# Performance work log

Hardware: AMD Instinct MI355X
Metric: run time of the kernel (lower is better)

Reference implementation:

```python
import jax, jax.numpy as jnp
import numpy as np

EMBED_DIM = 768
NUM_HEADS = 12
NUM_BOND_TYPES = 4
NEG_INF = -1e9


def setup_inputs() -> dict:
    key = jax.random.key(0)
    ks = jax.random.split(key, 8)
    B, N, E = 32, 512, EMBED_DIM
    x = jax.random.normal(ks[0], (B, N, E), dtype=jnp.float32)
    adj = jax.random.randint(ks[1], (B, N, N), 0, 2, dtype=jnp.int32)
    bond = jax.random.randint(ks[2], (B, N, N), 0, NUM_BOND_TYPES + 1, dtype=jnp.int32)
    # nn.Linear(E, 3E): weight (3E, E), bias (3E)
    lim_qkv = 1.0 / np.sqrt(E)
    qkv_w = jax.random.uniform(ks[3], (3 * E, E), minval=-lim_qkv, maxval=lim_qkv, dtype=jnp.float32)
    qkv_b = jax.random.uniform(ks[4], (3 * E,), minval=-lim_qkv, maxval=lim_qkv, dtype=jnp.float32)
    out_w = jax.random.uniform(ks[5], (E, E), minval=-lim_qkv, maxval=lim_qkv, dtype=jnp.float32)
    out_b = jax.random.uniform(ks[6], (E,), minval=-lim_qkv, maxval=lim_qkv, dtype=jnp.float32)
    # nn.Embedding(num_bond_types+1, 1), padding_idx=0 -> row 0 is zero
    bond_table = jax.random.normal(ks[7], (NUM_BOND_TYPES + 1, 1), dtype=jnp.float32)
    bond_table = bond_table.at[0].set(0.0)
    return {"x": x, "adj": adj, "bond": bond, "num_heads": NUM_HEADS,
            "qkv_w": qkv_w, "qkv_b": qkv_b, "out_w": out_w, "out_b": out_b,
            "bond_table": bond_table}


def reference(x, adj, bond, num_heads, qkv_w, qkv_b, out_w, out_b, bond_table):
    B, N, E = x.shape
    hd = E // num_heads
    scale = hd ** -0.5
    # enforce padding_idx=0 semantics
    bond_table = bond_table.at[0].set(0.0)
    qkv = x @ qkv_w.T + qkv_b                      # (B, N, 3E)
    qkv = qkv.reshape(B, N, 3, num_heads, hd).transpose(2, 0, 3, 1, 4)
    q, k, v = qkv[0], qkv[1], qkv[2]               # (B, h, N, hd)
    attn = jnp.einsum('bhnd,bhmd->bhnm', q, k) * scale
    attn = attn + adj.astype(x.dtype)[:, None, :, :]
    bond_bias = bond_table[bond, 0]                # (B, N, N) embedding gather
    attn = attn + bond_bias[:, None, :, :]
    attn = jnp.where(attn == 0, NEG_INF, attn)     # masked_fill(attn == 0)
    attn = jax.nn.softmax(attn, axis=-1)
    out = jnp.einsum('bhnm,bhmd->bhnd', attn, v)   # (B, h, N, hd)
    out = out.transpose(0, 2, 1, 3).reshape(B, N, E)
    return out @ out_w.T + out_b
```

## Files before the change

### kernel.cpp

```cpp
#include <hip/hip_runtime.h>
#include <hip/hip_bf16.h>

typedef __attribute__((ext_vector_type(8))) short short8;
typedef __attribute__((ext_vector_type(4))) float f32x4;
typedef __attribute__((ext_vector_type(4))) unsigned int uint4v;
typedef __attribute__((ext_vector_type(4))) int int4v;

#define MFMA16(a,b,c) __builtin_amdgcn_mfma_f32_16x16x32_bf16((a),(b),(c),0,0,0)

#define GLOAD_LDS16(g, l) \
    __builtin_amdgcn_global_load_lds((const __attribute__((address_space(1))) void*)(g), \
                                     (__attribute__((address_space(3))) void*)(l), 16, 0, 0)

__device__ __forceinline__ unsigned short f2bf(float f){
    union { float f; unsigned int u; } c; c.f = f;
    unsigned int u = c.u;
    u = (u + 0x7fffu + ((u >> 16) & 1u)) >> 16;
    return (unsigned short)u;
}
__device__ __forceinline__ float bf2f(unsigned short s){
    union { unsigned int u; float f; } c; c.u = ((unsigned int)s) << 16;
    return c.f;
}

__device__ __forceinline__ void tsplit(float f, unsigned short &h, unsigned short &l){
    unsigned int u = __builtin_bit_cast(unsigned int, f);
    float hi = __builtin_bit_cast(float, u & 0xffff0000u);
    h = (unsigned short)(u >> 16);
    l = (unsigned short)(__builtin_bit_cast(unsigned int, f - hi) >> 16);
}


__global__ void pack_x_kernel(const float* __restrict__ x, unsigned int* __restrict__ img){
    int tid = blockIdx.x * 256 + threadIdx.x;
    int m = tid / 96, grp = tid - m * 96;
    const float* src = x + (size_t)m * 768 + grp * 8;
    f32x4 v0 = ((const f32x4*)src)[0];
    f32x4 v1 = ((const f32x4*)src)[1];
    short8 h8, l8;
    #pragma unroll
    for (int j = 0; j < 4; ++j){
        unsigned short hh, ll;
        tsplit(v0[j], hh, ll); h8[j]   = (short)hh; l8[j]   = (short)ll;
        tsplit(v1[j], hh, ll); h8[4+j] = (short)hh; l8[4+j] = (short)ll;
    }
    int mt = m >> 7, row = m & 127, kt = grp >> 2, gi = grp & 3;
    int sw = (row & 7) << 4;
    char* bp = (char*)img + ((size_t)(mt*24 + kt))*16384 + row*128;
    *(short8*)(bp + ((gi*32     ) ^ sw)) = h8;
    *(short8*)(bp + ((gi*32 + 16) ^ sw)) = l8;
}

__global__ void pack_w_kernel(const float* __restrict__ wsrc, unsigned int* __restrict__ img, int total){
    int tid = blockIdx.x * 256 + threadIdx.x;
    if (tid >= total) return;
    int n = tid / 96, grp = tid - n * 96;
    const float* src = wsrc + (size_t)n * 768 + grp * 8;
    f32x4 v0 = ((const f32x4*)src)[0];
    f32x4 v1 = ((const f32x4*)src)[1];
    short8 h8, l8;
    #pragma unroll
    for (int j = 0; j < 4; ++j){
        unsigned short hh = f2bf(v0[j]);
        h8[j] = (short)hh; l8[j] = (short)f2bf(v0[j] - bf2f(hh));
        hh = f2bf(v1[j]);
        h8[4+j] = (short)hh; l8[4+j] = (short)f2bf(v1[j] - bf2f(hh));
    }
    int jt = n >> 7, row = n & 127, kt = grp >> 2, gi = grp & 3;
    int sw = (row & 7) << 4;
    char* bp = (char*)img + ((size_t)(jt*24 + kt))*16384 + row*128;
    *(short8*)(bp + ((gi*32     ) ^ sw)) = h8;
    *(short8*)(bp + ((gi*32 + 16) ^ sw)) = l8;
}

__global__ void bias_kernel(const int* __restrict__ adj, const int* __restrict__ bond,
                            const float* __restrict__ table, float* __restrict__ biasC, int n4){
    int i = blockIdx.x * 256 + threadIdx.x;
    if (i >= n4) return;
    int4v a  = ((const int4v*)adj)[i];
    int4v bd = ((const int4v*)bond)[i];
    const float t1 = table[1], t2 = table[2], t3 = table[3], t4 = table[4];
    f32x4 o;
    #pragma unroll
    for (int j = 0; j < 4; ++j){
        int bv = bd[j];
        float tb = (bv == 1) ? t1 : (bv == 2) ? t2 : (bv == 3) ? t3 : (bv == 4) ? t4 : 0.0f;
        o[j] = (float)a[j] + tb;
    }
    ((f32x4*)biasC)[i] = o;
}

template<int EMODE>
__global__ __launch_bounds__(256, 3)
void gemm_img(const unsigned int* __restrict__ Aimg, const unsigned int* __restrict__ Bimg,
              const float* __restrict__ bias, int NT, int RPX,
              float* __restrict__ C, int N,
              char* __restrict__ qo, char* __restrict__ ko, char* __restrict__ vo)
{
    __shared__ unsigned int lds[8192];

    const int lin = blockIdx.x;
    const int xcd = lin & 7, idx = lin >> 3;
    const int grp  = idx / (RPX * 6);
    const int rem  = idx - grp * (RPX * 6);
    const int rowL = rem / 6, c6 = rem - rowL * 6;
    const int colT = grp * 6 + c6;
    const int mt = xcd * RPX + rowL;
    const int m0 = mt << 7, j0 = colT << 7;

    const int t = threadIdx.x, l = t & 63, w = t >> 6;
    const int c = l & 15, g = l >> 4;
    const int wr = (w >> 1) * 64, wc2 = (w & 1) * 64;

    const unsigned int* Ablk = Aimg + (size_t)mt   * NT * 4096;
    const unsigned int* Bblk = Bimg + (size_t)colT * NT * 4096;

    f32x4 acc[4][4] = {};

    for (int kt = 0; kt < NT; ++kt){
        const unsigned int* As = Ablk + kt*4096 + t*4;
        const unsigned int* Bs = Bblk + kt*4096 + t*4;
        unsigned int* Ad = lds + t*4;
        unsigned int* Bd = lds + 4096 + t*4;
        #pragma unroll
        for (int i = 0; i < 4; ++i){
            GLOAD_LDS16(As + i*1024, Ad + i*1024);
            GLOAD_LDS16(Bs + i*1024, Bd + i*1024);
        }
        __syncthreads();

        short8 bh[4], bl[4];
        #pragma unroll
        for (int fc = 0; fc < 4; ++fc){
            int row = wc2 + fc*16 + c;
            int sw = (row & 7) << 4;
            const char* p = (const char*)(lds + 4096) + row*128;
            bh[fc] = *(const short8*)(p + ((g*32     ) ^ sw));
            bl[fc] = *(const short8*)(p + ((g*32 + 16) ^ sw));
        }
        #pragma unroll
        for (int fr = 0; fr < 4; ++fr){
            int row = wr + fr*16 + c;
            int sw = (row & 7) << 4;
            const char* p = (const char*)lds + row*128;
            short8 ah = *(const short8*)(p + ((g*32     ) ^ sw));
            short8 al = *(const short8*)(p + ((g*32 + 16) ^ sw));
            __builtin_amdgcn_s_setprio(1);
            #pragma unroll
            for (int fc = 0; fc < 4; ++fc){
                acc[fr][fc] = MFMA16(ah, bh[fc], acc[fr][fc]);
                acc[fr][fc] = MFMA16(ah, bl[fc], acc[fr][fc]);
                acc[fr][fc] = MFMA16(al, bh[fc], acc[fr][fc]);
            }
            __builtin_amdgcn_s_setprio(0);
        }
        __syncthreads();
    }

    #pragma unroll
    for (int fr = 0; fr < 4; ++fr){
        #pragma unroll
        for (int fc = 0; fc < 4; ++fc){
            #pragma unroll
            for (int r = 0; r < 4; ++r){
                int m = m0 + wr + fr*16 + g*4 + r;
                int j = j0 + wc2 + fc*16 + c;
                float val = acc[fr][fc][r] + bias[j];
                if constexpr (EMODE == 0){
                    C[(size_t)m * N + j] = val;
                } else {
                    int sec = j / 768;
                    int off = j - sec * 768;
                    int head = off >> 6, d = off & 63;
                    int bb = m >> 9, n = m & 511;
                    int bh2 = bb * 12 + head;
                    unsigned short hh, ll;
                    tsplit(val, hh, ll);
                    if (sec == 0) {
                        char* p = qo + ((size_t)bh2*512 + n)*256 + (d>>3)*32 + (d&7)*2;
                        *(unsigned short*)(p     ) = hh;
                        *(unsigned short*)(p + 16) = ll;
                    } else if (sec == 1) {
                        int row = n & 63;
                        int ksw = (((row & 7) + (((row >> 3) & 3) << 1)) & 7) << 4;
                        char* p = ko + (size_t)(bh2*8 + (n>>6))*16384 + row*256;
                        *(unsigned short*)(p + ((((d>>3)*32)     ) ^ ksw) + (d&7)*2) = hh;
                        *(unsigned short*)(p + ((((d>>3)*32) + 16) ^ ksw) + (d&7)*2) = ll;
                    } else {
                        int col = n & 63, sw = (d & 7) << 4;
                        char* p = vo + (size_t)(bh2*8 + (n>>6))*16384 + d*256;
                        *(unsigned short*)(p + ((((col>>3)*32)     ) ^ sw) + (col&7)*2) = hh;
                        *(unsigned short*)(p + ((((col>>3)*32) + 16) ^ sw) + (col&7)*2) = ll;
                    }
                }
            }
        }
    }
}

__global__ __launch_bounds__(256, 4)
void attn_kernel(const char* __restrict__ qb,
                 const unsigned int* __restrict__ kimg,
                 const unsigned int* __restrict__ vimg,
                 const float* __restrict__ biasC,
                 char* __restrict__ oimg)
{
    __shared__ unsigned int Kt[4096];
    __shared__ unsigned int Vt[4096];

    const int lin = blockIdx.x;
    const int xcd = lin & 7, m_ = lin >> 3;
    const int bgrp = m_ / 96, r_ = m_ - bgrp * 96;
    const int b = (bgrp << 3) | xcd;
    const int h = r_ >> 3, qt = r_ & 7;
    const int bh = b * 12 + h, q0 = qt * 64;

    const int t = threadIdx.x, l = t & 63, w = t >> 6;
    const int c = l & 15, g = l >> 4;

    short8 qh[2], ql[2];
    {
        int qrow = q0 + w*16 + c;
        const char* qp = qb + ((size_t)bh*512 + qrow)*256;
        #pragma unroll
        for (int ks = 0; ks < 2; ++ks){
            qh[ks] = *(const short8*)(qp + ks*128 + g*32);
            ql[ks] = *(const short8*)(qp + ks*128 + g*32 + 16);
        }
    }

    f32x4 O[4] = {};
    float m_run = -3e38f, l_run = 0.0f;

    const float* biasRow = biasC + ((size_t)b * 512 + (q0 + w*16 + c)) * 512;

    for (int kt = 0; kt < 8; ++kt){
        {
            const unsigned int* kg = kimg + (size_t)(bh*8 + kt)*4096 + t*4;
            const unsigned int* vg = vimg + (size_t)(bh*8 + kt)*4096 + t*4;
            #pragma unroll
            for (int i = 0; i < 4; ++i){
                GLOAD_LDS16(kg + i*1024, &Kt[t*4 + i*1024]);
                GLOAD_LDS16(vg + i*1024, &Vt[t*4 + i*1024]);
            }
        }

        f32x4 bia[4];
        #pragma unroll
        for (int fc = 0; fc < 4; ++fc){
            int keyb = kt*64 + (fc>>1)*32 + g*8 + ((fc&1)<<2);
            bia[fc] = *(const f32x4*)(biasRow + keyb);
        }
        __syncthreads();

        f32x4 S[4] = {};
        #pragma unroll
        for (int fc = 0; fc < 4; ++fc){
            int row = (fc>>1)*32 + ((c>>2)<<3) + ((fc&1)<<2) + (c&3);
            int ksw = (((row & 7) + (((row >> 3) & 3) << 1)) & 7) << 4;
            const char* kp = (const char*)Kt + row*256;
            short8 kbh0 = *(const short8*)(kp + ((g*32           ) ^ ksw));
            short8 kbl0 = *(const short8*)(kp + ((g*32 + 16      ) ^ ksw));
            short8 kbh1 = *(const short8*)(kp + ((128 + g*32     ) ^ ksw));
            short8 kbl1 = *(const short8*)(kp + ((128 + g*32 + 16) ^ ksw));
            __builtin_amdgcn_s_setprio(1);
            S[fc] = MFMA16(kbh0, qh[0], S[fc]);
            S[fc] = MFMA16(kbl0, qh[0], S[fc]);
            S[fc] = MFMA16(kbh0, ql[0], S[fc]);
            S[fc] = MFMA16(kbh1, qh[1], S[fc]);
            S[fc] = MFMA16(kbl1, qh[1], S[fc]);
            S[fc] = MFMA16(kbh1, ql[1], S[fc]);
            __builtin_amdgcn_s_setprio(0);
        }

        float p[4][4];
        float pmax = -3e38f;
        #pragma unroll
        for (int fc = 0; fc < 4; ++fc){
            #pragma unroll
            for (int r = 0; r < 4; ++r){
                float val = fmaf(S[fc][r], 0.125f, bia[fc][r]);
                if (val == 0.0f) val = -1e9f;
                p[fc][r] = val;
                pmax = fmaxf(pmax, val);
            }
        }
        pmax = fmaxf(pmax, __shfl_xor(pmax, 16));
        pmax = fmaxf(pmax, __shfl_xor(pmax, 32));
        float mn = fmaxf(m_run, pmax);
        float corr = __expf(m_run - mn);
        float rs = 0.0f;
        #pragma unroll
        for (int fc = 0; fc < 4; ++fc){
            #pragma unroll
            for (int r = 0; r < 4; ++r){
                float e = __expf(p[fc][r] - mn);
                p[fc][r] = e;
                rs += e;
            }
        }
        rs += __shfl_xor(rs, 16);
        rs += __shfl_xor(rs, 32);
        l_run = l_run * corr + rs;
        m_run = mn;

        #pragma unroll
        for (int r = 0; r < 4; ++r){
            float cr = __shfl(corr, (l & 48) | (g*4 + r));
            O[0][r] *= cr; O[1][r] *= cr; O[2][r] *= cr; O[3][r] *= cr;
        }

        #pragma unroll
        for (int ks = 0; ks < 2; ++ks){
            uint4v ph, plo;
            #pragma unroll
            for (int j = 0; j < 4; ++j){
                const int fc = 2*ks + (j >> 1);
                const int r0 = (j & 1) * 2;
                float a  = p[fc][r0], bq = p[fc][r0 + 1];
                unsigned int ua = __builtin_bit_cast(unsigned int, a);
                unsigned int ub = __builtin_bit_cast(unsigned int, bq);
                float ra = a  - __builtin_bit_cast(float, ua & 0xffff0000u);
                float rb = bq - __builtin_bit_cast(float, ub & 0xffff0000u);
                ph[j]  = __builtin_amdgcn_perm(ub, ua, 0x07060302u);
                plo[j] = __builtin_amdgcn_perm(__builtin_bit_cast(unsigned int, rb),
                                               __builtin_bit_cast(unsigned int, ra), 0x07060302u);
            }
            short8 pah = __builtin_bit_cast(short8, ph);
            short8 pal = __builtin_bit_cast(short8, plo);
            #pragma unroll
            for (int hf = 0; hf < 4; ++hf){
                int row = hf*16 + c;
                int sw = (row & 7) << 4;
                const char* vp = (const char*)Vt + row*256;
                short8 vbh = *(const short8*)(vp + ((ks*128 + g*32     ) ^ sw));
                short8 vbl = *(const short8*)(vp + ((ks*128 + g*32 + 16) ^ sw));
                __builtin_amdgcn_s_setprio(1);
                O[hf] = MFMA16(pah, vbh, O[hf]);
                O[hf] = MFMA16(pah, vbl, O[hf]);
                O[hf] = MFMA16(pal, vbh, O[hf]);
                __builtin_amdgcn_s_setprio(0);
            }
        }
        __syncthreads();
    }

    float linv = 1.0f / l_run;
    #pragma unroll
    for (int r = 0; r < 4; ++r){
        float inv = __shfl(linv, (l & 48) | (g*4 + r));
        int m = b*512 + q0 + w*16 + g*4 + r;
        int mt = m >> 7, mrow2 = m & 127;
        int swz = (mrow2 & 7) << 4;
        char* rowp = oimg + ((size_t)mt*24)*16384 + (size_t)mrow2*128;
        #pragma unroll
        for (int hf = 0; hf < 4; ++hf){
            int e = h*64 + hf*16 + c;
            int kt2 = e >> 5, gi = (e >> 3) & 3, pos = e & 7;
            unsigned short hh, ll;
            tsplit(O[hf][r] * inv, hh, ll);
            char* pp = rowp + (size_t)kt2*16384;
            *(unsigned short*)(pp + (((gi*32)     ) ^ swz) + pos*2) = hh;
            *(unsigned short*)(pp + (((gi*32) + 16) ^ swz) + pos*2) = ll;
        }
    }
}

extern "C" void kernel_launch(void* const* d_in, const int* in_sizes, int n_in,
                              void* d_out, int out_size, void* d_ws, size_t ws_size,
                              hipStream_t stream)
{
    const float* x     = (const float*)d_in[0];
    const int*   adj   = (const int*)d_in[1];
    const int*   bond  = (const int*)d_in[2];
    const float* qkv_w = (const float*)d_in[4];
    const float* qkv_b = (const float*)d_in[5];
    const float* out_w = (const float*)d_in[6];
    const float* out_b = (const float*)d_in[7];
    const float* btab  = (const float*)d_in[8];
    float* out = (float*)d_out;

    const size_t QKV = 12582912;
    unsigned int* q   = (unsigned int*)d_ws;
    unsigned int* k   = q  + QKV;
    unsigned int* vt  = k  + QKV;
    unsigned int* r1  = vt + QKV;
    unsigned int* w2i = r1 + QKV;
    unsigned int* r2  = w2i + 589824;
    unsigned int* w1i = r2;
    float* biasC      = (float*)r2;

    dim3 blk(256);
    pack_w_kernel<<<dim3(864), blk, 0, stream>>>(qkv_w, w1i, 2304*96);
    pack_w_kernel<<<dim3(288), blk, 0, stream>>>(out_w, w2i, 768*96);
    pack_x_kernel<<<dim3(6144), blk, 0, stream>>>(x, r1);

    gemm_img<1><<<dim3(2304), blk, 0, stream>>>(r1, w1i, qkv_b, 24, 16,
                                                nullptr, 2304, (char*)q, (char*)k, (char*)vt);

    bias_kernel<<<dim3(8192), blk, 0, stream>>>(adj, bond, btab, biasC, (32*512*512)/4);

    attn_kernel<<<dim3(3072), blk, 0, stream>>>((const char*)q, k, vt, biasC, (char*)r1);

    gemm_img<0><<<dim3(768), blk, 0, stream>>>(r1, w2i, out_b, 24, 16,
                                               out, 768, nullptr, nullptr, nullptr);
}
```

Baseline: 389.3 us.

## Enlarge GEMM tiles to 256x256 with 512 threads and double-buffered LDS prefetch

Reworks the split-bf16 GEMM kernel to use 256x256 output tiles per 512-thread block with 128KB of dynamic LDS. The next K-tile is loaded into a second buffer while the current one is consumed by MFMAs, interleaved across four sub-phases with barriers. The aim is to hide global-to-LDS latency and raise data reuse per load. In exchange, occupancy drops to one block per CU and register pressure rises from the 8x4 accumulator array. The grid is also much smaller (576 and 192 blocks), which risks poor CU fill for the output projection.

```diff
diff --git a/kernel.cpp b/kernel.cpp
--- a/kernel.cpp
+++ b/kernel.cpp
@@ -91,80 +91,117 @@
 }
 
 template<int EMODE>
-__global__ __launch_bounds__(256, 3)
+__global__ __launch_bounds__(512, 1)
 void gemm_img(const unsigned int* __restrict__ Aimg, const unsigned int* __restrict__ Bimg,
-              const float* __restrict__ bias, int NT, int RPX,
+              const float* __restrict__ bias, int NT, int NCOL,
               float* __restrict__ C, int N,
               char* __restrict__ qo, char* __restrict__ ko, char* __restrict__ vo)
 {
-    __shared__ unsigned int lds[8192];
+    extern __shared__ unsigned int lds[];
 
     const int lin = blockIdx.x;
     const int xcd = lin & 7, idx = lin >> 3;
-    const int grp  = idx / (RPX * 6);
-    const int rem  = idx - grp * (RPX * 6);
-    const int rowL = rem / 6, c6 = rem - rowL * 6;
-    const int colT = grp * 6 + c6;
-    const int mt = xcd * RPX + rowL;
-    const int m0 = mt << 7, j0 = colT << 7;
+    const int rowL = idx / NCOL, colT = idx - rowL * NCOL;
+    const int bm = xcd * 8 + rowL;
+    const int m0 = bm << 8, j0 = colT << 8;
 
     const int t = threadIdx.x, l = t & 63, w = t >> 6;
     const int c = l & 15, g = l >> 4;
-    const int wr = (w >> 1) * 64, wc2 = (w & 1) * 64;
-
-    const unsigned int* Ablk = Aimg + (size_t)mt   * NT * 4096;
-    const unsigned int* Bblk = Bimg + (size_t)colT * NT * 4096;
-
-    f32x4 acc[4][4] = {};
+    const int wr2 = (w >> 2) * 128;
+    const int wc4 = (w & 3) * 64;
+
+    const unsigned int* Ab0 = Aimg + (size_t)(bm*2    ) * NT * 4096;
+    const unsigned int* Ab1 = Aimg + (size_t)(bm*2 + 1) * NT * 4096;
+    const unsigned int* Bb0 = Bimg + (size_t)(colT*2    ) * NT * 4096;
+    const unsigned int* Bb1 = Bimg + (size_t)(colT*2 + 1) * NT * 4096;
+
+    const int Aoff = (w >> 2) * 16384;
+    const int Boff = (2 + ((w & 3) >> 1)) * 16384;
+    const int rBbase = (w & 1) * 64;
+
+    f32x4 acc[8][4] = {};
+
+    {
+        const unsigned int* s0 = Ab0 + t*4;
+        const unsigned int* s1 = Ab1 + t*4;
+        const unsigned int* s2 = Bb0 + t*4;
+        const unsigned int* s3 = Bb1 + t*4;
+        unsigned int* d = lds + t*4;
+        GLOAD_LDS16(s0,        d        ); GLOAD_LDS16(s0 + 2048, d + 2048 );
+        GLOAD_LDS16(s1,        d + 4096 ); GLOAD_LDS16(s1 + 2048, d + 6144 );
+        GLOAD_LDS16(s2,        d + 8192 ); GLOAD_LDS16(s2 + 2048, d + 10240);
+        GLOAD_LDS16(s3,        d + 12288); GLOAD_LDS16(s3 + 2048, d + 14336);
+    }
+    asm volatile("s_waitcnt vmcnt(0)" ::: "memory");
+    __builtin_amdgcn_s_barrier();
 
     for (int kt = 0; kt < NT; ++kt){
-        const unsigned int* As = Ablk + kt*4096 + t*4;
-        const unsigned int* Bs = Bblk + kt*4096 + t*4;
-        unsigned int* Ad = lds + t*4;
-        unsigned int* Bd = lds + 4096 + t*4;
-        #pragma unroll
-        for (int i = 0; i < 4; ++i){
-            GLOAD_LDS16(As + i*1024, Ad + i*1024);
-            GLOAD_LDS16(Bs + i*1024, Bd + i*1024);
-        }
-        __syncthreads();
+        const char* bufb = (const char*)lds + (kt & 1) * 65536;
+        unsigned int* bufn = lds + ((kt & 1) ^ 1) * 16384;
+        const bool pre = (kt + 1 < NT);
 
         short8 bh[4], bl[4];
         #pragma unroll
+        for (int p = 0; p < 4; ++p){
+            short8 ah[2], al[2];
+            #pragma unroll
+            for (int i = 0; i < 2; ++i){
+                int r = (2*p + i)*16 + c;
+                int sw = (r & 7) << 4;
+                const char* pa = bufb + Aoff + r*128;
+                ah[i] = *(const short8*)(pa + ((g*32     ) ^ sw));
+                al[i] = *(const short8*)(pa + ((g*32 + 16) ^ sw));
+            }
+            if (p == 0){
+                #pragma unroll
+                for (int fc = 0; fc < 4; ++fc){
+                    int r = rBbase + fc*16 + c;
+                    int sw = (r & 7) << 4;
+                    const char* pb = bufb + Boff + r*128;
+                    bh[fc] = *(const short8*)(pb + ((g*32     ) ^ sw));
+                    bl[fc] = *(const short8*)(pb + ((g*32 + 16) ^ sw));
+                }
+                if (pre){
+                    const unsigned int* s0 = Ab0 + (kt+1)*4096 + t*4;
+                    const unsigned int* s1 = Ab1 + (kt+1)*4096 + t*4;
+                    unsigned int* d = bufn + t*4;
+                    GLOAD_LDS16(s0,        d       ); GLOAD_LDS16(s0 + 2048, d + 2048);
+                    GLOAD_LDS16(s1,        d + 4096); GLOAD_LDS16(s1 + 2048, d + 6144);
+                }
+            }
+            if (p == 1 && pre){
+                const unsigned int* s2 = Bb0 + (kt+1)*4096 + t*4;
+                const unsigned int* s3 = Bb1 + (kt+1)*4096 + t*4;
+                unsigned int* d = bufn + t*4;
+                GLOAD_LDS16(s2,        d + 8192 ); GLOAD_LDS16(s2 + 2048, d + 10240);
+                GLOAD_LDS16(s3,        d + 12288); GLOAD_LDS16(s3 + 2048, d + 14336);
+            }
+            __builtin_amdgcn_s_barrier();
+            __builtin_amdgcn_s_setprio(1);
+            #pragma unroll
+            for (int i = 0; i < 2; ++i){
+                #pragma unroll
+                for (int fc = 0; fc < 4; ++fc){
+                    acc[2*p+i][fc] = MFMA16(ah[i], bh[fc], acc[2*p+i][fc]);
+                    acc[2*p+i][fc] = MFMA16(ah[i], bl[fc], acc[2*p+i][fc]);
+                    acc[2*p+i][fc] = MFMA16(al[i], bh[fc], acc[2*p+i][fc]);
+                }
+            }
+            __builtin_amdgcn_s_setprio(0);
+            if (p == 3)
+                asm volatile("s_waitcnt vmcnt(0)" ::: "memory");
+            __builtin_amdgcn_s_barrier();
+        }
+    }
+
+    #pragma unroll
+    for (int fr = 0; fr < 8; ++fr){
+        #pragma unroll
         for (int fc = 0; fc < 4; ++fc){
-            int row = wc2 + fc*16 + c;
-            int sw = (row & 7) << 4;
-            const char* p = (const char*)(lds + 4096) + row*128;
-            bh[fc] = *(const short8*)(p + ((g*32     ) ^ sw));
-            bl[fc] = *(const short8*)(p + ((g*32 + 16) ^ sw));
-        }
-        #pragma unroll
-        for (int fr = 0; fr < 4; ++fr){
-            int row = wr + fr*16 + c;
-            int sw = (row & 7) << 4;
-            const char* p = (const char*)lds + row*128;
-            short8 ah = *(const short8*)(p + ((g*32     ) ^ sw));
-            short8 al = *(const short8*)(p + ((g*32 + 16) ^ sw));
-            __builtin_amdgcn_s_setprio(1);
-            #pragma unroll
-            for (int fc = 0; fc < 4; ++fc){
-                acc[fr][fc] = MFMA16(ah, bh[fc], acc[fr][fc]);
-                acc[fr][fc] = MFMA16(ah, bl[fc], acc[fr][fc]);
-                acc[fr][fc] = MFMA16(al, bh[fc], acc[fr][fc]);
-            }
-            __builtin_amdgcn_s_setprio(0);
-        }
-        __syncthreads();
-    }
-
-    #pragma unroll
-    for (int fr = 0; fr < 4; ++fr){
-        #pragma unroll
-        for (int fc = 0; fc < 4; ++fc){
             #pragma unroll
             for (int r = 0; r < 4; ++r){
-                int m = m0 + wr + fr*16 + g*4 + r;
-                int j = j0 + wc2 + fc*16 + c;
+                int m = m0 + wr2 + fr*16 + g*4 + r;
+                int j = j0 + wc4 + fc*16 + c;
                 float val = acc[fr][fc][r] + bias[j];
                 if constexpr (EMODE == 0){
                     C[(size_t)m * N + j] = val;
@@ -395,13 +432,13 @@
     pack_w_kernel<<<dim3(288), blk, 0, stream>>>(out_w, w2i, 768*96);
     pack_x_kernel<<<dim3(6144), blk, 0, stream>>>(x, r1);
 
-    gemm_img<1><<<dim3(2304), blk, 0, stream>>>(r1, w1i, qkv_b, 24, 16,
-                                                nullptr, 2304, (char*)q, (char*)k, (char*)vt);
+    gemm_img<1><<<dim3(576), dim3(512), 131072, stream>>>(
+        r1, w1i, qkv_b, 24, 9, nullptr, 2304, (char*)q, (char*)k, (char*)vt);
 
     bias_kernel<<<dim3(8192), blk, 0, stream>>>(adj, bond, btab, biasC, (32*512*512)/4);
 
     attn_kernel<<<dim3(3072), blk, 0, stream>>>((const char*)q, k, vt, biasC, (char*)r1);
 
-    gemm_img<0><<<dim3(768), blk, 0, stream>>>(r1, w2i, out_b, 24, 16,
-                                               out, 768, nullptr, nullptr, nullptr);
-}
+    gemm_img<0><<<dim3(192), dim3(512), 131072, stream>>>(
+        r1, w2i, out_b, 24, 3, out, 768, nullptr, nullptr, nullptr);
+}
```

New measurement: 444.7 us. 14.2% more time.

## Process 128 query rows per attention block to reuse K/V tiles

Applied to the files above, without the earlier changes.

Each attention workgroup now handles 128 queries instead of 64: every wave processes two 16-row query sub-tiles against the same K/V LDS tiles, which halves the number of blocks and the total K/V global-to-LDS traffic and sync count. Register pressure rises (double S, O, P state), so attention's launch bound drops to 3 waves per SIMD, while the GEMM's bound is raised to 4. The swapped occupancy hints may trade spills or latency hiding against the reuse gain.

```diff
diff --git a/kernel.cpp b/kernel.cpp
--- a/kernel.cpp
+++ b/kernel.cpp
@@ -91,7 +91,7 @@
 }
 
 template<int EMODE>
-__global__ __launch_bounds__(256, 3)
+__global__ __launch_bounds__(256, 4)
 void gemm_img(const unsigned int* __restrict__ Aimg, const unsigned int* __restrict__ Bimg,
               const float* __restrict__ bias, int NT, int RPX,
               float* __restrict__ C, int N,
@@ -198,7 +198,7 @@
     }
 }
 
-__global__ __launch_bounds__(256, 4)
+__global__ __launch_bounds__(256, 3)
 void attn_kernel(const char* __restrict__ qb,
                  const unsigned int* __restrict__ kimg,
                  const unsigned int* __restrict__ vimg,
@@ -210,29 +210,32 @@
 
     const int lin = blockIdx.x;
     const int xcd = lin & 7, m_ = lin >> 3;
-    const int bgrp = m_ / 96, r_ = m_ - bgrp * 96;
+    const int bgrp = m_ / 48, r_ = m_ - bgrp * 48;
     const int b = (bgrp << 3) | xcd;
-    const int h = r_ >> 3, qt = r_ & 7;
-    const int bh = b * 12 + h, q0 = qt * 64;
+    const int h = r_ >> 2, qt = r_ & 3;
+    const int bh = b * 12 + h, q0 = qt * 128;
 
     const int t = threadIdx.x, l = t & 63, w = t >> 6;
     const int c = l & 15, g = l >> 4;
 
-    short8 qh[2], ql[2];
-    {
-        int qrow = q0 + w*16 + c;
+    short8 qh[2][2], ql[2][2];
+    #pragma unroll
+    for (int qk = 0; qk < 2; ++qk){
+        int qrow = q0 + w*32 + qk*16 + c;
         const char* qp = qb + ((size_t)bh*512 + qrow)*256;
         #pragma unroll
         for (int ks = 0; ks < 2; ++ks){
-            qh[ks] = *(const short8*)(qp + ks*128 + g*32);
-            ql[ks] = *(const short8*)(qp + ks*128 + g*32 + 16);
-        }
-    }
-
-    f32x4 O[4] = {};
-    float m_run = -3e38f, l_run = 0.0f;
-
-    const float* biasRow = biasC + ((size_t)b * 512 + (q0 + w*16 + c)) * 512;
+            qh[qk][ks] = *(const short8*)(qp + ks*128 + g*32);
+            ql[qk][ks] = *(const short8*)(qp + ks*128 + g*32 + 16);
+        }
+    }
+
+    f32x4 O[2][4] = {};
+    float m_run[2] = {-3e38f, -3e38f};
+    float l_run[2] = {0.f, 0.f};
+
+    const float* biasRow0 = biasC + ((size_t)b * 512 + (q0 + w*32 + c)) * 512;
+    const float* biasRow1 = biasRow0 + (size_t)16 * 512;
 
     for (int kt = 0; kt < 8; ++kt){
         {
@@ -245,15 +248,16 @@
             }
         }
 
-        f32x4 bia[4];
+        f32x4 bia[2][4];
         #pragma unroll
         for (int fc = 0; fc < 4; ++fc){
             int keyb = kt*64 + (fc>>1)*32 + g*8 + ((fc&1)<<2);
-            bia[fc] = *(const f32x4*)(biasRow + keyb);
+            bia[0][fc] = *(const f32x4*)(biasRow0 + keyb);
+            bia[1][fc] = *(const f32x4*)(biasRow1 + keyb);
         }
         __syncthreads();
 
-        f32x4 S[4] = {};
+        f32x4 S[2][4] = {};
         #pragma unroll
         for (int fc = 0; fc < 4; ++fc){
             int row = (fc>>1)*32 + ((c>>2)<<3) + ((fc&1)<<2) + (c&3);
@@ -264,70 +268,82 @@
             short8 kbh1 = *(const short8*)(kp + ((128 + g*32     ) ^ ksw));
             short8 kbl1 = *(const short8*)(kp + ((128 + g*32 + 16) ^ ksw));
             __builtin_amdgcn_s_setprio(1);
-            S[fc] = MFMA16(kbh0, qh[0], S[fc]);
-            S[fc] = MFMA16(kbl0, qh[0], S[fc]);
-            S[fc] = MFMA16(kbh0, ql[0], S[fc]);
-            S[fc] = MFMA16(kbh1, qh[1], S[fc]);
-            S[fc] = MFMA16(kbl1, qh[1], S[fc]);
-            S[fc] = MFMA16(kbh1, ql[1], S[fc]);
+            #pragma unroll
+            for (int qk = 0; qk < 2; ++qk){
+                S[qk][fc] = MFMA16(kbh0, qh[qk][0], S[qk][fc]);
+                S[qk][fc] = MFMA16(kbl0, qh[qk][0], S[qk][fc]);
+                S[qk][fc] = MFMA16(kbh0, ql[qk][0], S[qk][fc]);
+                S[qk][fc] = MFMA16(kbh1, qh[qk][1], S[qk][fc]);
+                S[qk][fc] = MFMA16(kbl1, qh[qk][1], S[qk][fc]);
+                S[qk][fc] = MFMA16(kbh1, ql[qk][1], S[qk][fc]);
+            }
             __builtin_amdgcn_s_setprio(0);
         }
 
-        float p[4][4];
-        float pmax = -3e38f;
-        #pragma unroll
-        for (int fc = 0; fc < 4; ++fc){
+        short8 pah[2][2], pal[2][2];
+        #pragma unroll
+        for (int qk = 0; qk < 2; ++qk){
+            float p[4][4];
+            float pmax = -3e38f;
+            #pragma unroll
+            for (int fc = 0; fc < 4; ++fc){
+                #pragma unroll
+                for (int r = 0; r < 4; ++r){
+                    float val = fmaf(S[qk][fc][r], 0.125f, bia[qk][fc][r]);
+                    if (val == 0.0f) val = -1e9f;
+                    p[fc][r] = val;
+                    pmax = fmaxf(pmax, val);
+                }
+            }
+            pmax = fmaxf(pmax, __shfl_xor(pmax, 16));
+            pmax = fmaxf(pmax, __shfl_xor(pmax, 32));
+            float mn = fmaxf(m_run[qk], pmax);
+            float corr = __expf(m_run[qk] - mn);
+            float rs = 0.0f;
+            #pragma unroll
+            for (int fc = 0; fc < 4; ++fc){
+                #pragma unroll
+                for (int r = 0; r < 4; ++r){
+                    float e = __expf(p[fc][r] - mn);
+                    p[fc][r] = e;
+                    rs += e;
+                }
+            }
+            rs += __shfl_xor(rs, 16);
+            rs += __shfl_xor(rs, 32);
+            l_run[qk] = l_run[qk] * corr + rs;
+            m_run[qk] = mn;
+
             #pragma unroll
             for (int r = 0; r < 4; ++r){
-                float val = fmaf(S[fc][r], 0.125f, bia[fc][r]);
-                if (val == 0.0f) val = -1e9f;
-                p[fc][r] = val;
-                pmax = fmaxf(pmax, val);
-            }
-        }
-        pmax = fmaxf(pmax, __shfl_xor(pmax, 16));
-        pmax = fmaxf(pmax, __shfl_xor(pmax, 32));
-        float mn = fmaxf(m_run, pmax);
-        float corr = __expf(m_run - mn);
-        float rs = 0.0f;
-        #pragma unroll
-        for (int fc = 0; fc < 4; ++fc){
-            #pragma unroll
-            for (int r = 0; r < 4; ++r){
-                float e = __expf(p[fc][r] - mn);
-                p[fc][r] = e;
-                rs += e;
-            }
-        }
-        rs += __shfl_xor(rs, 16);
-        rs += __shfl_xor(rs, 32);
-        l_run = l_run * corr + rs;
-        m_run = mn;
-
-        #pragma unroll
-        for (int r = 0; r < 4; ++r){
-            float cr = __shfl(corr, (l & 48) | (g*4 + r));
-            O[0][r] *= cr; O[1][r] *= cr; O[2][r] *= cr; O[3][r] *= cr;
+                float cr = __shfl(corr, (l & 48) | (g*4 + r));
+                O[qk][0][r] *= cr; O[qk][1][r] *= cr;
+                O[qk][2][r] *= cr; O[qk][3][r] *= cr;
+            }
+
+            #pragma unroll
+            for (int ks = 0; ks < 2; ++ks){
+                uint4v ph, plo;
+                #pragma unroll
+                for (int j = 0; j < 4; ++j){
+                    const int fc = 2*ks + (j >> 1);
+                    const int r0 = (j & 1) * 2;
+                    float a  = p[fc][r0], bq = p[fc][r0 + 1];
+                    unsigned int ua = __builtin_bit_cast(unsigned int, a);
+                    unsigned int ub = __builtin_bit_cast(unsigned int, bq);
+                    float ra = a  - __builtin_bit_cast(float, ua & 0xffff0000u);
+                    float rb = bq - __builtin_bit_cast(float, ub & 0xffff0000u);
+                    ph[j]  = __builtin_amdgcn_perm(ub, ua, 0x07060302u);
+                    plo[j] = __builtin_amdgcn_perm(__builtin_bit_cast(unsigned int, rb),
+                                                   __builtin_bit_cast(unsigned int, ra), 0x07060302u);
+                }
+                pah[qk][ks] = __builtin_bit_cast(short8, ph);
+                pal[qk][ks] = __builtin_bit_cast(short8, plo);
+            }
         }
 
         #pragma unroll
         for (int ks = 0; ks < 2; ++ks){
-            uint4v ph, plo;
-            #pragma unroll
-            for (int j = 0; j < 4; ++j){
-                const int fc = 2*ks + (j >> 1);
-                const int r0 = (j & 1) * 2;
-                float a  = p[fc][r0], bq = p[fc][r0 + 1];
-                unsigned int ua = __builtin_bit_cast(unsigned int, a);
-                unsigned int ub = __builtin_bit_cast(unsigned int, bq);
-                float ra = a  - __builtin_bit_cast(float, ua & 0xffff0000u);
-                float rb = bq - __builtin_bit_cast(float, ub & 0xffff0000u);
-                ph[j]  = __builtin_amdgcn_perm(ub, ua, 0x07060302u);
-                plo[j] = __builtin_amdgcn_perm(__builtin_bit_cast(unsigned int, rb),
-                                               __builtin_bit_cast(unsigned int, ra), 0x07060302u);
-            }
-            short8 pah = __builtin_bit_cast(short8, ph);
-            short8 pal = __builtin_bit_cast(short8, plo);
             #pragma unroll
             for (int hf = 0; hf < 4; ++hf){
                 int row = hf*16 + c;
@@ -336,32 +352,38 @@
                 short8 vbh = *(const short8*)(vp + ((ks*128 + g*32     ) ^ sw));
                 short8 vbl = *(const short8*)(vp + ((ks*128 + g*32 + 16) ^ sw));
                 __builtin_amdgcn_s_setprio(1);
-                O[hf] = MFMA16(pah, vbh, O[hf]);
-                O[hf] = MFMA16(pah, vbl, O[hf]);
-                O[hf] = MFMA16(pal, vbh, O[hf]);
+                #pragma unroll
+                for (int qk = 0; qk < 2; ++qk){
+                    O[qk][hf] = MFMA16(pah[qk][ks], vbh, O[qk][hf]);
+                    O[qk][hf] = MFMA16(pah[qk][ks], vbl, O[qk][hf]);
+                    O[qk][hf] = MFMA16(pal[qk][ks], vbh, O[qk][hf]);
+                }
                 __builtin_amdgcn_s_setprio(0);
             }
         }
         __syncthreads();
     }
 
-    float linv = 1.0f / l_run;
-    #pragma unroll
-    for (int r = 0; r < 4; ++r){
-        float inv = __shfl(linv, (l & 48) | (g*4 + r));
-        int m = b*512 + q0 + w*16 + g*4 + r;
-        int mt = m >> 7, mrow2 = m & 127;
-        int swz = (mrow2 & 7) << 4;
-        char* rowp = oimg + ((size_t)mt*24)*16384 + (size_t)mrow2*128;
-        #pragma unroll
-        for (int hf = 0; hf < 4; ++hf){
-            int e = h*64 + hf*16 + c;
-            int kt2 = e >> 5, gi = (e >> 3) & 3, pos = e & 7;
-            unsigned short hh, ll;
-            tsplit(O[hf][r] * inv, hh, ll);
-            char* pp = rowp + (size_t)kt2*16384;
-            *(unsigned short*)(pp + (((gi*32)     ) ^ swz) + pos*2) = hh;
-            *(unsigned short*)(pp + (((gi*32) + 16) ^ swz) + pos*2) = ll;
+    #pragma unroll
+    for (int qk = 0; qk < 2; ++qk){
+        float linv = 1.0f / l_run[qk];
+        #pragma unroll
+        for (int r = 0; r < 4; ++r){
+            float inv = __shfl(linv, (l & 48) | (g*4 + r));
+            int m = b*512 + q0 + w*32 + qk*16 + g*4 + r;
+            int mt = m >> 7, mrow2 = m & 127;
+            int swz = (mrow2 & 7) << 4;
+            char* rowp = oimg + ((size_t)mt*24)*16384 + (size_t)mrow2*128;
+            #pragma unroll
+            for (int hf = 0; hf < 4; ++hf){
+                int e = h*64 + hf*16 + c;
+                int kt2 = e >> 5, gi = (e >> 3) & 3, pos = e & 7;
+                unsigned short hh, ll;
+                tsplit(O[qk][hf][r] * inv, hh, ll);
+                char* pp = rowp + (size_t)kt2*16384;
+                *(unsigned short*)(pp + (((gi*32)     ) ^ swz) + pos*2) = hh;
+                *(unsigned short*)(pp + (((gi*32) + 16) ^ swz) + pos*2) = ll;
+            }
         }
     }
 }
@@ -400,7 +422,7 @@
 
     bias_kernel<<<dim3(8192), blk, 0, stream>>>(adj, bond, btab, biasC, (32*512*512)/4);
 
-    attn_kernel<<<dim3(3072), blk, 0, stream>>>((const char*)q, k, vt, biasC, (char*)r1);
+    attn_kernel<<<dim3(1536), blk, 0, stream>>>((const char*)q, k, vt, biasC, (char*)r1);
 
     gemm_img<0><<<dim3(768), blk, 0, stream>>>(r1, w2i, out_b, 24, 16,
                                                out, 768, nullptr, nullptr, nullptr);
```

New measurement: 398.5 us. 2.4% more time.
